# Kernel tuning notes

Measured on AMD Instinct MI355X. Metric: run time of the kernel, lower is better.

## Reference

```python
import jax, jax.numpy as jnp
import numpy as np

HEADS = 4
HID = 128
NEG_SLOPE = 0.2
N_NODES = 20000
N_EDGES = 320000
N_GRAPHS = 64
IN_DIM = 12


def gat_layer(x, src, dst, W, a_src, a_dst, b, n):
    # PyG GATConv, heads=4, concat=False (mean over heads), add_self_loops handled by caller.
    h = (x @ W).reshape(n, HEADS, HID)                      # [N,H,C]
    e_src = jnp.einsum('nhc,hc->nh', h, a_src)              # [N,H]
    e_dst = jnp.einsum('nhc,hc->nh', h, a_dst)
    e = jax.nn.leaky_relu(e_src[src] + e_dst[dst], NEG_SLOPE)  # [E,H]
    m = jax.lax.stop_gradient(jax.ops.segment_max(e, dst, num_segments=n))
    ex = jnp.exp(e - m[dst])
    denom = jax.ops.segment_sum(ex, dst, num_segments=n)    # [N,H]
    alpha = ex / denom[dst]                                 # edge softmax over incoming edges
    out = jax.ops.segment_sum(alpha[:, :, None] * h[src], dst, num_segments=n)  # [N,H,C]
    return out.mean(axis=1) + b                             # concat=False -> head mean, then bias


def setup_inputs() -> dict:
    key = jax.random.key(0)
    ks = jax.random.split(key, 20)
    def glorot(k, shape):
        lim = float(np.sqrt(6.0 / (shape[0] + shape[-1])))
        return jax.random.uniform(k, shape, jnp.float32, -lim, lim)
    inp = {
        'x': jax.random.normal(ks[0], (N_NODES, IN_DIM), jnp.float32),
        'edge_index': jax.random.randint(ks[1], (2, N_EDGES), 0, N_NODES, jnp.int64 if jax.config.jax_enable_x64 else jnp.int32),
        'batch': jnp.sort(jax.random.randint(ks[2], (N_NODES,), 0, N_GRAPHS)),
        'batch_size_tensor': jax.random.uniform(ks[3], (N_GRAPHS, 1), jnp.float32),
        # GAT layer 1
        'W1': glorot(ks[4], (IN_DIM, HEADS * HID)), 'as1': glorot(ks[5], (HEADS, HID)),
        'ad1': glorot(ks[6], (HEADS, HID)), 'b1': jnp.zeros((HID,), jnp.float32),
        # GAT layer 2
        'W2': glorot(ks[7], (HID, HEADS * HID)), 'as2': glorot(ks[8], (HEADS, HID)),
        'ad2': glorot(ks[9], (HEADS, HID)), 'b2': jnp.zeros((HID,), jnp.float32),
        # GAT layer 3
        'W3': glorot(ks[10], (HID, HEADS * HID)), 'as3': glorot(ks[11], (HEADS, HID)),
        'ad3': glorot(ks[12], (HEADS, HID)), 'b3': jnp.zeros((HID,), jnp.float32),
        # MLP: (128+1)->128->64->2
        'M1': glorot(ks[13], (HID + 1, HID)), 'mb1': jnp.zeros((HID,), jnp.float32),
        'M2': glorot(ks[14], (HID, HID // 2)), 'mb2': jnp.zeros((HID // 2,), jnp.float32),
        'M3': glorot(ks[15], (HID // 2, 2)), 'mb3': jnp.zeros((2,), jnp.float32),
    }
    return inp


def reference(x, edge_index, batch, batch_size_tensor,
              W1, as1, ad1, b1, W2, as2, ad2, b2, W3, as3, ad3, b3,
              M1, mb1, M2, mb2, M3, mb3):
    n = x.shape[0]
    loops = jnp.arange(n, dtype=edge_index.dtype)
    src = jnp.concatenate([edge_index[0], loops])   # add_self_loops=True (PyG default)
    dst = jnp.concatenate([edge_index[1], loops])
    h = jax.nn.relu(gat_layer(x, src, dst, W1, as1, ad1, b1, n))
    h = jax.nn.relu(gat_layer(h, src, dst, W2, as2, ad2, b2, n))
    h = jax.nn.relu(gat_layer(h, src, dst, W3, as3, ad3, b3, n))
    # global mean pool over graphs
    g = batch_size_tensor.shape[0]
    sums = jax.ops.segment_sum(h, batch, num_segments=g)
    cnts = jax.ops.segment_sum(jnp.ones((n,), h.dtype), batch, num_segments=g)
    pooled = sums / jnp.maximum(cnts, 1.0)[:, None]          # [G,128]
    bs = jnp.log1p(batch_size_tensor)                        # [G,1]
    z = jnp.concatenate([pooled, bs], axis=1)                # [G,129]
    z = jax.nn.relu(z @ M1 + mb1)                            # dropout(0.2) is identity at eval
    z = jax.nn.relu(z @ M2 + mb2)
    return z @ M3 + mb3                                      # [G,2]
```

## Files before the change

### kernel.cpp

```cpp
#include <hip/hip_runtime.h>
#include <hip/hip_bf16.h>
#include <math.h>

#define NN 20000
#define NE 320000
#define ET (NE + NN)
#define NG 64
#define HEADS 4
#define HID 128
#define OUTC (HEADS * HID)
#define SLOPE 0.2f

__device__ __forceinline__ float lrelu(float v) { return v > 0.f ? v : SLOPE * v; }

__global__ void k_hist(const int* __restrict__ ei, int* __restrict__ deg) {
  int e = blockIdx.x * blockDim.x + threadIdx.x;
  if (e >= ET) return;
  int dst = (e < NE) ? ei[NE + e] : (e - NE);
  atomicAdd(&deg[dst], 1);
}

__global__ void k_scan(const int* __restrict__ deg, int* __restrict__ row_start,
                       int* __restrict__ cursor) {
  __shared__ int sums[1024];
  int tid = threadIdx.x;
  const int PER = (NN + 1023) / 1024;
  int base = tid * PER;
  int local = 0;
  for (int i = 0; i < PER; ++i) { int idx = base + i; if (idx < NN) local += deg[idx]; }
  sums[tid] = local;
  __syncthreads();
  for (int off = 1; off < 1024; off <<= 1) {
    int v = (tid >= off) ? sums[tid - off] : 0;
    __syncthreads();
    sums[tid] += v;
    __syncthreads();
  }
  int run = sums[tid] - local;
  for (int i = 0; i < PER; ++i) {
    int idx = base + i;
    if (idx < NN) { row_start[idx] = run; cursor[idx] = run; run += deg[idx]; }
  }
  if (tid == 1023) row_start[NN] = sums[1023];
}

__global__ void k_scatter(const int* __restrict__ ei, int* __restrict__ cursor,
                          int* __restrict__ csr_src) {
  int e = blockIdx.x * blockDim.x + threadIdx.x;
  if (e >= ET) return;
  int src, dst;
  if (e < NE) { src = ei[e]; dst = ei[NE + e]; }
  else        { src = e - NE; dst = src; }
  int pos = atomicAdd(&cursor[dst], 1);
  csr_src[pos] = src;
}

__global__ void k_watt3(const float* __restrict__ W1, const float* __restrict__ as1,
                        const float* __restrict__ ad1, const float* __restrict__ W2,
                        const float* __restrict__ as2, const float* __restrict__ ad2,
                        const float* __restrict__ W3, const float* __restrict__ as3,
                        const float* __restrict__ ad3, float* __restrict__ watt1,
                        float* __restrict__ watt2, float* __restrict__ watt3) {
  int b = blockIdx.x;
  const float *W, *as, *ad;
  float* wo;
  int k;
  if (b < 12)       { k = b;       W = W1; as = as1; ad = ad1; wo = watt1; }
  else if (b < 140) { k = b - 12;  W = W2; as = as2; ad = ad2; wo = watt2; }
  else              { k = b - 140; W = W3; as = as3; ad = ad3; wo = watt3; }
  int tid = threadIdx.x;
  int t = tid & 7, h = t & 3;
  int c0 = (tid >> 3) * 4;
  const float* av = (t < 4 ? as : ad) + h * HID;
  const float* wr = W + (size_t)k * OUTC + h * HID;
  float4 wv = *reinterpret_cast<const float4*>(&wr[c0]);
  float4 a4 = *reinterpret_cast<const float4*>(&av[c0]);
  float p = wv.x * a4.x + wv.y * a4.y + wv.z * a4.z + wv.w * a4.w;
  __shared__ float lp[32][8];
  lp[tid >> 3][t] = p;
  __syncthreads();
  if (tid < 8) {
    float s = 0.f;
    for (int cc = 0; cc < 32; ++cc) s += lp[cc][tid];
    wo[k * 8 + tid] = s;
  }
}

__global__ void k_esd1(const float* __restrict__ x, const float* __restrict__ watt,
                       float* __restrict__ es, float* __restrict__ ed) {
  int n = blockIdx.x * blockDim.x + threadIdx.x;
  if (n >= NN) return;
  float xr[12];
#pragma unroll
  for (int k = 0; k < 12; ++k) xr[k] = x[(size_t)n * 12 + k];
#pragma unroll
  for (int t = 0; t < 8; ++t) {
    float acc = 0.f;
#pragma unroll
    for (int k = 0; k < 12; ++k) acc += xr[k] * watt[k * 8 + t];
    if (t < 4) es[n * 4 + t] = acc;
    else       ed[n * 4 + (t - 4)] = acc;
  }
}

__global__ void __launch_bounds__(256) k_esd128(
    const float* __restrict__ x, const float* __restrict__ watt,
    float* __restrict__ es, float* __restrict__ ed) {
  __shared__ float sw[HID * 8];
  int tid = threadIdx.x;
  for (int i = tid; i < HID * 8; i += 256) sw[i] = watt[i];
  __syncthreads();
  int local = tid >> 3;
  int t = tid & 7;
  int n = blockIdx.x * 32 + local;
  const float4* xr = reinterpret_cast<const float4*>(&x[(size_t)n * HID]);
  float acc = 0.f;
#pragma unroll 8
  for (int kq = 0; kq < 32; ++kq) {
    float4 xv = xr[kq];
    acc += xv.x * sw[(kq * 4 + 0) * 8 + t] + xv.y * sw[(kq * 4 + 1) * 8 + t]
         + xv.z * sw[(kq * 4 + 2) * 8 + t] + xv.w * sw[(kq * 4 + 3) * 8 + t];
  }
  if (t < 4) es[n * 4 + t] = acc;
  else       ed[n * 4 + (t - 4)] = acc;
}

__global__ void __launch_bounds__(256, 4) k_aggf(
    const float* __restrict__ x, const float* __restrict__ es,
    const float* __restrict__ ed, const int* __restrict__ row_start,
    const int* __restrict__ csr_src, float* __restrict__ z) {
  __shared__ float sal[4][256];
  int wid = threadIdx.x >> 6;
  int lane = threadIdx.x & 63;
  int n = blockIdx.x * 4 + wid;
  int start = row_start[n];
  int deg = row_start[n + 1] - start;
  const int* sp = csr_src + start;
  float4 edv = *reinterpret_cast<const float4*>(&ed[(size_t)n * 4]);
  int c = lane * 2;
  float2 a0c = make_float2(0.f, 0.f), a1c = make_float2(0.f, 0.f);
  float2 a2c = make_float2(0.f, 0.f), a3c = make_float2(0.f, 0.f);
  float d0 = 0.f, d1 = 0.f, d2 = 0.f, d3 = 0.f;
  for (int cb = 0; cb < deg; cb += 64) {
    int m = min(64, deg - cb);
    {
      int kk = cb + ((lane < m) ? lane : (m - 1));
      int s = sp[kk];
      float4 e4 = *reinterpret_cast<const float4*>(&es[(size_t)s * 4]);
      float4 ex;
      ex.x = __expf(lrelu(e4.x + edv.x));
      ex.y = __expf(lrelu(e4.y + edv.y));
      ex.z = __expf(lrelu(e4.z + edv.z));
      ex.w = __expf(lrelu(e4.w + edv.w));
      if (lane < m) {
        *reinterpret_cast<float4*>(&sal[wid][lane * 4]) = ex;
        d0 += ex.x; d1 += ex.y; d2 += ex.z; d3 += ex.w;
      }
    }
    asm volatile("s_waitcnt lgkmcnt(0)" ::: "memory");
    int j = 0;
    for (; j + 4 <= m; j += 4) {
      float4 q0 = *reinterpret_cast<const float4*>(&sal[wid][(j + 0) * 4]);
      float4 q1 = *reinterpret_cast<const float4*>(&sal[wid][(j + 1) * 4]);
      float4 q2 = *reinterpret_cast<const float4*>(&sal[wid][(j + 2) * 4]);
      float4 q3 = *reinterpret_cast<const float4*>(&sal[wid][(j + 3) * 4]);
      int s0 = sp[cb + j + 0], s1 = sp[cb + j + 1];
      int s2 = sp[cb + j + 2], s3 = sp[cb + j + 3];
      float2 x0 = *reinterpret_cast<const float2*>(&x[(size_t)s0 * HID + c]);
      float2 x1 = *reinterpret_cast<const float2*>(&x[(size_t)s1 * HID + c]);
      float2 x2 = *reinterpret_cast<const float2*>(&x[(size_t)s2 * HID + c]);
      float2 x3 = *reinterpret_cast<const float2*>(&x[(size_t)s3 * HID + c]);
      a0c.x += q0.x * x0.x; a0c.y += q0.x * x0.y;
      a1c.x += q0.y * x0.x; a1c.y += q0.y * x0.y;
      a2c.x += q0.z * x0.x; a2c.y += q0.z * x0.y;
      a3c.x += q0.w * x0.x; a3c.y += q0.w * x0.y;
      a0c.x += q1.x * x1.x; a0c.y += q1.x * x1.y;
      a1c.x += q1.y * x1.x; a1c.y += q1.y * x1.y;
      a2c.x += q1.z * x1.x; a2c.y += q1.z * x1.y;
      a3c.x += q1.w * x1.x; a3c.y += q1.w * x1.y;
      a0c.x += q2.x * x2.x; a0c.y += q2.x * x2.y;
      a1c.x += q2.y * x2.x; a1c.y += q2.y * x2.y;
      a2c.x += q2.z * x2.x; a2c.y += q2.z * x2.y;
      a3c.x += q2.w * x2.x; a3c.y += q2.w * x2.y;
      a0c.x += q3.x * x3.x; a0c.y += q3.x * x3.y;
      a1c.x += q3.y * x3.x; a1c.y += q3.y * x3.y;
      a2c.x += q3.z * x3.x; a2c.y += q3.z * x3.y;
      a3c.x += q3.w * x3.x; a3c.y += q3.w * x3.y;
    }
    for (; j < m; ++j) {
      float4 q = *reinterpret_cast<const float4*>(&sal[wid][j * 4]);
      int s = sp[cb + j];
      float2 xv = *reinterpret_cast<const float2*>(&x[(size_t)s * HID + c]);
      a0c.x += q.x * xv.x; a0c.y += q.x * xv.y;
      a1c.x += q.y * xv.x; a1c.y += q.y * xv.y;
      a2c.x += q.z * xv.x; a2c.y += q.z * xv.y;
      a3c.x += q.w * xv.x; a3c.y += q.w * xv.y;
    }
  }
#pragma unroll
  for (int off = 1; off < 64; off <<= 1) {
    d0 += __shfl_xor(d0, off);
    d1 += __shfl_xor(d1, off);
    d2 += __shfl_xor(d2, off);
    d3 += __shfl_xor(d3, off);
  }
  float i0 = 0.25f / d0, i1 = 0.25f / d1, i2 = 0.25f / d2, i3 = 0.25f / d3;
  a0c.x *= i0; a0c.y *= i0;
  a1c.x *= i1; a1c.y *= i1;
  a2c.x *= i2; a2c.y *= i2;
  a3c.x *= i3; a3c.y *= i3;
  float* zr = z + (size_t)n * OUTC;
  *reinterpret_cast<float2*>(&zr[0 * HID + c]) = a0c;
  *reinterpret_cast<float2*>(&zr[1 * HID + c]) = a1c;
  *reinterpret_cast<float2*>(&zr[2 * HID + c]) = a2c;
  *reinterpret_cast<float2*>(&zr[3 * HID + c]) = a3c;
}

__global__ void __launch_bounds__(256, 4) k_aggf1(
    const float* __restrict__ x, const float* __restrict__ es,
    const float* __restrict__ ed, const int* __restrict__ row_start,
    const int* __restrict__ csr_src, float* __restrict__ z1) {
  __shared__ float sal[4][256];
  int wid = threadIdx.x >> 6;
  int lane = threadIdx.x & 63;
  int n = blockIdx.x * 4 + wid;
  int start = row_start[n];
  int deg = row_start[n + 1] - start;
  const int* sp = csr_src + start;
  float4 edv = *reinterpret_cast<const float4*>(&ed[(size_t)n * 4]);
  int h = lane >> 4;
  int cr = lane & 15;
  int cc = cr < 12 ? cr : 11;
  float acc = 0.f;
  float d0 = 0.f, d1 = 0.f, d2 = 0.f, d3 = 0.f;
  for (int cb = 0; cb < deg; cb += 64) {
    int m = min(64, deg - cb);
    {
      int kk = cb + ((lane < m) ? lane : (m - 1));
      int s = sp[kk];
      float4 e4 = *reinterpret_cast<const float4*>(&es[(size_t)s * 4]);
      float4 ex;
      ex.x = __expf(lrelu(e4.x + edv.x));
      ex.y = __expf(lrelu(e4.y + edv.y));
      ex.z = __expf(lrelu(e4.z + edv.z));
      ex.w = __expf(lrelu(e4.w + edv.w));
      if (lane < m) {
        *reinterpret_cast<float4*>(&sal[wid][lane * 4]) = ex;
        d0 += ex.x; d1 += ex.y; d2 += ex.z; d3 += ex.w;
      }
    }
    asm volatile("s_waitcnt lgkmcnt(0)" ::: "memory");
    int j = 0;
    for (; j + 4 <= m; j += 4) {
      float ah0 = sal[wid][(j + 0) * 4 + h];
      float ah1 = sal[wid][(j + 1) * 4 + h];
      float ah2 = sal[wid][(j + 2) * 4 + h];
      float ah3 = sal[wid][(j + 3) * 4 + h];
      int s0 = sp[cb + j + 0], s1 = sp[cb + j + 1];
      int s2 = sp[cb + j + 2], s3 = sp[cb + j + 3];
      float x0 = x[(size_t)s0 * 12 + cc];
      float x1 = x[(size_t)s1 * 12 + cc];
      float x2 = x[(size_t)s2 * 12 + cc];
      float x3 = x[(size_t)s3 * 12 + cc];
      acc += ah0 * x0 + ah1 * x1 + ah2 * x2 + ah3 * x3;
    }
    for (; j < m; ++j) {
      float ah = sal[wid][j * 4 + h];
      int s = sp[cb + j];
      acc += ah * x[(size_t)s * 12 + cc];
    }
  }
#pragma unroll
  for (int off = 1; off < 64; off <<= 1) {
    d0 += __shfl_xor(d0, off);
    d1 += __shfl_xor(d1, off);
    d2 += __shfl_xor(d2, off);
    d3 += __shfl_xor(d3, off);
  }
  float dh = (h == 0) ? d0 : (h == 1) ? d1 : (h == 2) ? d2 : d3;
  float ivh = 0.25f / dh;
  if (cr < 12) z1[(size_t)n * 48 + h * 12 + cr] = acc * ivh;
}

template <int KTOT, int KH, int BK>
__global__ void k_gemm_full(const float* __restrict__ z, const float* __restrict__ W,
                            const float* __restrict__ bias, float* __restrict__ xout) {
  const int BM = 64, BN = 64;
  __shared__ float sAT[BK][BM + 4];
  __shared__ float sB[BK][BN];
  int tid = threadIdx.x;
  int r0 = blockIdx.y * BM;
  int cb = blockIdx.x * BN;
  int tx = tid & 15, ty = tid >> 4;
  int m0 = ty * 4, n0 = tx * 4;
  float acc[4][4] = {};
  for (int k0 = 0; k0 < KTOT; k0 += BK) {
    const int AF4 = BM * BK / 4;
    for (int idx = tid; idx < AF4; idx += 256) {
      int r = idx / (BK / 4);
      int kq = idx % (BK / 4);
      int row = r0 + r;
      float4 v = make_float4(0.f, 0.f, 0.f, 0.f);
      if (row < NN) v = *reinterpret_cast<const float4*>(&z[(size_t)row * KTOT + k0 + kq * 4]);
      sAT[kq * 4 + 0][r] = v.x;
      sAT[kq * 4 + 1][r] = v.y;
      sAT[kq * 4 + 2][r] = v.z;
      sAT[kq * 4 + 3][r] = v.w;
    }
    const int BF4 = BK * BN / 4;
    for (int idx = tid; idx < BF4; idx += 256) {
      int kr = idx / 16, nq = idx & 15;
      int kk = k0 + kr;
      int h = kk / KH, k = kk % KH;
      float4 v = *reinterpret_cast<const float4*>(&W[(size_t)k * OUTC + h * HID + cb + nq * 4]);
      *reinterpret_cast<float4*>(&sB[kr][nq * 4]) = v;
    }
    __syncthreads();
#pragma unroll 4
    for (int kk = 0; kk < BK; ++kk) {
      float4 a = *reinterpret_cast<const float4*>(&sAT[kk][m0]);
      float4 b = *reinterpret_cast<const float4*>(&sB[kk][n0]);
      acc[0][0] += a.x * b.x; acc[0][1] += a.x * b.y; acc[0][2] += a.x * b.z; acc[0][3] += a.x * b.w;
      acc[1][0] += a.y * b.x; acc[1][1] += a.y * b.y; acc[1][2] += a.y * b.z; acc[1][3] += a.y * b.w;
      acc[2][0] += a.z * b.x; acc[2][1] += a.z * b.y; acc[2][2] += a.z * b.z; acc[2][3] += a.z * b.w;
      acc[3][0] += a.w * b.x; acc[3][1] += a.w * b.y; acc[3][2] += a.w * b.z; acc[3][3] += a.w * b.w;
    }
    __syncthreads();
  }
  float4 bv = *reinterpret_cast<const float4*>(&bias[cb + n0]);
#pragma unroll
  for (int i = 0; i < 4; ++i) {
    int row = r0 + m0 + i;
    if (row < NN) {
      float4 o;
      o.x = fmaxf(acc[i][0] + bv.x, 0.f);
      o.y = fmaxf(acc[i][1] + bv.y, 0.f);
      o.z = fmaxf(acc[i][2] + bv.z, 0.f);
      o.w = fmaxf(acc[i][3] + bv.w, 0.f);
      *reinterpret_cast<float4*>(&xout[(size_t)row * HID + cb + n0]) = o;
    }
  }
}

template <int KTOT, int KH, int BK, int KCH>
__global__ void k_gemm_ks(const float* __restrict__ z, const float* __restrict__ W,
                          float* __restrict__ part) {
  const int BM = 64, BN = 128;
  __shared__ float sAT[BK][BM + 4];
  __shared__ float sB[BK][BN];
  int tid = threadIdx.x;
  int r0 = blockIdx.y * BM;
  int kc = blockIdx.z;
  int tx = tid & 15, ty = tid >> 4;
  int m0 = ty * 4, n0 = tx * 4;
  float acc0[4][4] = {};
  float acc1[4][4] = {};
  for (int k0 = kc * KCH; k0 < (kc + 1) * KCH; k0 += BK) {
    const int AF4 = BM * BK / 4;
    for (int idx = tid; idx < AF4; idx += 256) {
      int r = idx / (BK / 4);
      int kq = idx % (BK / 4);
      int row = r0 + r;
      float4 v = make_float4(0.f, 0.f, 0.f, 0.f);
      if (row < NN) v = *reinterpret_cast<const float4*>(&z[(size_t)row * KTOT + k0 + kq * 4]);
      sAT[kq * 4 + 0][r] = v.x;
      sAT[kq * 4 + 1][r] = v.y;
      sAT[kq * 4 + 2][r] = v.z;
      sAT[kq * 4 + 3][r] = v.w;
    }
    const int BF4 = BK * BN / 4;
    for (int idx = tid; idx < BF4; idx += 256) {
      int kr = idx >> 5, nq = idx & 31;
      int kk = k0 + kr;
      int h = kk / KH, k = kk % KH;
      float4 v = *reinterpret_cast<const float4*>(&W[(size_t)k * OUTC + h * HID + nq * 4]);
      *reinterpret_cast<float4*>(&sB[kr][nq * 4]) = v;
    }
    __syncthreads();
#pragma unroll 4
    for (int kk = 0; kk < BK; ++kk) {
      float4 a = *reinterpret_cast<const float4*>(&sAT[kk][m0]);
      float4 b0 = *reinterpret_cast<const float4*>(&sB[kk][n0]);
      float4 b1 = *reinterpret_cast<const float4*>(&sB[kk][64 + n0]);
      acc0[0][0] += a.x * b0.x; acc0[0][1] += a.x * b0.y; acc0[0][2] += a.x * b0.z; acc0[0][3] += a.x * b0.w;
      acc0[1][0] += a.y * b0.x; acc0[1][1] += a.y * b0.y; acc0[1][2] += a.y * b0.z; acc0[1][3] += a.y * b0.w;
      acc0[2][0] += a.z * b0.x; acc0[2][1] += a.z * b0.y; acc0[2][2] += a.z * b0.z; acc0[2][3] += a.z * b0.w;
      acc0[3][0] += a.w * b0.x; acc0[3][1] += a.w * b0.y; acc0[3][2] += a.w * b0.z; acc0[3][3] += a.w * b0.w;
      acc1[0][0] += a.x * b1.x; acc1[0][1] += a.x * b1.y; acc1[0][2] += a.x * b1.z; acc1[0][3] += a.x * b1.w;
      acc1[1][0] += a.y * b1.x; acc1[1][1] += a.y * b1.y; acc1[1][2] += a.y * b1.z; acc1[1][3] += a.y * b1.w;
      acc1[2][0] += a.z * b1.x; acc1[2][1] += a.z * b1.y; acc1[2][2] += a.z * b1.z; acc1[2][3] += a.z * b1.w;
      acc1[3][0] += a.w * b1.x; acc1[3][1] += a.w * b1.y; acc1[3][2] += a.w * b1.z; acc1[3][3] += a.w * b1.w;
    }
    __syncthreads();
  }
#pragma unroll
  for (int i = 0; i < 4; ++i) {
    int row = r0 + m0 + i;
    if (row < NN) {
      float4 v0 = make_float4(acc0[i][0], acc0[i][1], acc0[i][2], acc0[i][3]);
      float4 v1 = make_float4(acc1[i][0], acc1[i][1], acc1[i][2], acc1[i][3]);
      float* pr = &part[((size_t)kc * NN + row) * HID];
      *reinterpret_cast<float4*>(&pr[n0]) = v0;
      *reinterpret_cast<float4*>(&pr[64 + n0]) = v1;
    }
  }
}

template <int POOL, int NKC>
__global__ void k_epi(const float* __restrict__ part, const float* __restrict__ bias,
                      const int* __restrict__ batch, float* __restrict__ xout,
                      float* __restrict__ gsums) {
  int tid = threadIdx.x;
  int row = blockIdx.x * 2 + (tid >> 7);
  int c = tid & 127;
  float o = bias[c];
#pragma unroll
  for (int kc = 0; kc < NKC; ++kc)
    o += part[((size_t)kc * NN + row) * HID + c];
  o = fmaxf(o, 0.f);
  if (POOL) {
    atomicAdd(&gsums[(size_t)batch[row] * HID + c], o);
  } else {
    xout[(size_t)row * HID + c] = o;
  }
}

__global__ void k_mlp(const float* __restrict__ sums, const int* __restrict__ batch,
                      const float* __restrict__ bst, const float* __restrict__ M1,
                      const float* __restrict__ mb1, const float* __restrict__ M2,
                      const float* __restrict__ mb2, const float* __restrict__ M3,
                      const float* __restrict__ mb3, float* __restrict__ out) {
  int g = blockIdx.x, tid = threadIdx.x;
  int lo = 0, hi = NN;
  while (lo < hi) { int mid = (lo + hi) >> 1; if (batch[mid] < g) lo = mid + 1; else hi = mid; }
  int s = lo;
  lo = s; hi = NN;
  while (lo < hi) { int mid = (lo + hi) >> 1; if (batch[mid] < g + 1) lo = mid + 1; else hi = mid; }
  int e = lo;
  float cnt = (float)(e - s);
  float pooled = sums[g * HID + tid] / fmaxf(cnt, 1.f);
  __shared__ float z[HID + 1];
  __shared__ float z1[HID];
  __shared__ float z2[64];
  z[tid] = pooled;
  if (tid == 0) z[HID] = log1pf(bst[g]);
  __syncthreads();
  float a1 = mb1[tid];
  for (int k = 0; k < HID + 1; ++k) a1 += z[k] * M1[k * HID + tid];
  z1[tid] = a1 > 0.f ? a1 : 0.f;
  __syncthreads();
  if (tid < 64) {
    float a2 = mb2[tid];
    for (int k = 0; k < HID; ++k) a2 += z1[k] * M2[k * 64 + tid];
    z2[tid] = a2 > 0.f ? a2 : 0.f;
  }
  __syncthreads();
  if (tid < 2) {
    float a3 = mb3[tid];
    for (int k = 0; k < 64; ++k) a3 += z2[k] * M3[k * 2 + tid];
    out[g * 2 + tid] = a3;
  }
}

extern "C" void kernel_launch(void* const* d_in, const int* in_sizes, int n_in,
                              void* d_out, int out_size, void* d_ws, size_t ws_size,
                              hipStream_t stream) {
  const float* x   = (const float*)d_in[0];
  const int*   ei  = (const int*)d_in[1];
  const int*   bat = (const int*)d_in[2];
  const float* bst = (const float*)d_in[3];
  const float* W1 = (const float*)d_in[4];
  const float* as1 = (const float*)d_in[5];
  const float* ad1 = (const float*)d_in[6];
  const float* b1 = (const float*)d_in[7];
  const float* W2 = (const float*)d_in[8];
  const float* as2 = (const float*)d_in[9];
  const float* ad2 = (const float*)d_in[10];
  const float* b2 = (const float*)d_in[11];
  const float* W3 = (const float*)d_in[12];
  const float* as3 = (const float*)d_in[13];
  const float* ad3 = (const float*)d_in[14];
  const float* b3 = (const float*)d_in[15];
  const float* M1 = (const float*)d_in[16];
  const float* mb1 = (const float*)d_in[17];
  const float* M2 = (const float*)d_in[18];
  const float* mb2 = (const float*)d_in[19];
  const float* M3 = (const float*)d_in[20];
  const float* mb3 = (const float*)d_in[21];
  float* out = (float*)d_out;

  const bool use4 = ws_size >= (size_t)110 * 1024 * 1024;

  char* ws = (char*)d_ws;
  auto alloc = [&](size_t bytes) -> void* {
    void* p = (void*)ws;
    ws += (bytes + 255) & ~(size_t)255;
    return p;
  };
  float* z_buf  = (float*)alloc((size_t)NN * OUTC * 4);
  float* z1_buf = (float*)alloc((size_t)NN * 48 * 4);
  float* x_buf  = (float*)alloc((size_t)NN * HID * 4);
  float* e_src  = (float*)alloc((size_t)NN * 4 * 4);
  float* e_dst  = (float*)alloc((size_t)NN * 4 * 4);
  int*   deg    = (int*)alloc((size_t)NN * 4);
  int*   rowst  = (int*)alloc((size_t)(NN + 1) * 4);
  int*   cursor = (int*)alloc((size_t)NN * 4);
  int*   csr    = (int*)alloc((size_t)ET * 4);
  float* part   = (float*)alloc((size_t)(use4 ? 4 : 2) * NN * HID * 4);
  float* watt1  = (float*)alloc((size_t)12 * 8 * 4);
  float* watt2  = (float*)alloc((size_t)HID * 8 * 4);
  float* watt3  = (float*)alloc((size_t)HID * 8 * 4);
  float* gsums  = (float*)alloc((size_t)NG * HID * 4);

  hipMemsetAsync(deg, 0, (size_t)NN * 4, stream);
  hipMemsetAsync(gsums, 0, (size_t)NG * HID * 4, stream);
  k_hist<<<(ET + 255) / 256, 256, 0, stream>>>(ei, deg);
  k_scan<<<1, 1024, 0, stream>>>(deg, rowst, cursor);
  k_scatter<<<(ET + 255) / 256, 256, 0, stream>>>(ei, cursor, csr);
  k_watt3<<<268, 256, 0, stream>>>(W1, as1, ad1, W2, as2, ad2, W3, as3, ad3,
                                   watt1, watt2, watt3);

  dim3 pgrid(NN / 4);
  dim3 g1grid(2, (NN + 63) / 64);
  dim3 ks4grid(1, (NN + 63) / 64, 4);
  dim3 ks2grid(1, (NN + 63) / 64, 2);
  dim3 epigrid(NN / 2);
  k_esd1<<<(NN + 255) / 256, 256, 0, stream>>>(x, watt1, e_src, e_dst);
  k_aggf1<<<pgrid, 256, 0, stream>>>(x, e_src, e_dst, rowst, csr, z1_buf);
  k_gemm_full<48, 12, 48><<<g1grid, 256, 0, stream>>>(z1_buf, W1, b1, x_buf);
  k_esd128<<<NN / 32, 256, 0, stream>>>(x_buf, watt2, e_src, e_dst);
  k_aggf<<<pgrid, 256, 0, stream>>>(x_buf, e_src, e_dst, rowst, csr, z_buf);
  if (use4) {
    k_gemm_ks<512, 128, 32, 128><<<ks4grid, 256, 0, stream>>>(z_buf, W2, part);
    k_epi<0, 4><<<epigrid, 256, 0, stream>>>(part, b2, bat, x_buf, gsums);
  } else {
    k_gemm_ks<512, 128, 32, 256><<<ks2grid, 256, 0, stream>>>(z_buf, W2, part);
    k_epi<0, 2><<<epigrid, 256, 0, stream>>>(part, b2, bat, x_buf, gsums);
  }
  k_esd128<<<NN / 32, 256, 0, stream>>>(x_buf, watt3, e_src, e_dst);
  k_aggf<<<pgrid, 256, 0, stream>>>(x_buf, e_src, e_dst, rowst, csr, z_buf);
  if (use4) {
    k_gemm_ks<512, 128, 32, 128><<<ks4grid, 256, 0, stream>>>(z_buf, W3, part);
    k_epi<1, 4><<<epigrid, 256, 0, stream>>>(part, b3, bat, x_buf, gsums);
  } else {
    k_gemm_ks<512, 128, 32, 256><<<ks2grid, 256, 0, stream>>>(z_buf, W3, part);
    k_epi<1, 2><<<epigrid, 256, 0, stream>>>(part, b3, bat, x_buf, gsums);
  }
  k_mlp<<<NG, 128, 0, stream>>>(gsums, bat, bst, M1, mb1, M2, mb2, M3, mb3, out);
}
```

Measured before the change: 321.4 us.

## Fuse layer-2 epilogue with attention-score projection and add 8-way split-K path

Adds k_epi_esd, which reduces the split-K partials, applies bias and ReLU, writes the node features, and computes the per-node source/destination attention scores for the next layer from shared memory. This removes the separate k_esd128 launch and its re-read of x_buf. It also adds an 8-way split-K GEMM variant, chosen when the workspace is large enough, to raise parallelism at the cost of more partial-sum traffic in the epilogue. Only 8 of 256 threads per block do the score dot products, which may serialise the tail of that kernel.

```diff
diff --git a/kernel.cpp b/kernel.cpp
--- a/kernel.cpp
+++ b/kernel.cpp
@@ -425,6 +425,34 @@
   }
 }
 
+template <int NKC>
+__global__ void k_epi_esd(const float* __restrict__ part, const float* __restrict__ bias,
+                          float* __restrict__ xout, const float* __restrict__ watt,
+                          float* __restrict__ es, float* __restrict__ ed) {
+  __shared__ float sx[2][HID];
+  int tid = threadIdx.x;
+  int slot = tid >> 7;
+  int row = blockIdx.x * 2 + slot;
+  int c = tid & 127;
+  float o = bias[c];
+#pragma unroll
+  for (int kc = 0; kc < NKC; ++kc)
+    o += part[((size_t)kc * NN + row) * HID + c];
+  o = fmaxf(o, 0.f);
+  xout[(size_t)row * HID + c] = o;
+  sx[slot][c] = o;
+  __syncthreads();
+  int t = tid & 127;
+  if (t < 8) {
+    int r = blockIdx.x * 2 + slot;
+    float acc = 0.f;
+#pragma unroll 16
+    for (int k = 0; k < HID; ++k) acc += sx[slot][k] * watt[k * 8 + t];
+    if (t < 4) es[r * 4 + t] = acc;
+    else       ed[r * 4 + (t - 4)] = acc;
+  }
+}
+
 __global__ void k_mlp(const float* __restrict__ sums, const int* __restrict__ batch,
                       const float* __restrict__ bst, const float* __restrict__ M1,
                       const float* __restrict__ mb1, const float* __restrict__ M2,
@@ -489,7 +517,9 @@
   const float* mb3 = (const float*)d_in[21];
   float* out = (float*)d_out;
 
-  const bool use4 = ws_size >= (size_t)110 * 1024 * 1024;
+  const bool use8 = ws_size >= (size_t)170 * 1024 * 1024;
+  const bool use4 = !use8 && ws_size >= (size_t)110 * 1024 * 1024;
+  const int nkc = use8 ? 8 : (use4 ? 4 : 2);
 
   char* ws = (char*)d_ws;
   auto alloc = [&](size_t bytes) -> void* {
@@ -506,7 +536,7 @@
   int*   rowst  = (int*)alloc((size_t)(NN + 1) * 4);
   int*   cursor = (int*)alloc((size_t)NN * 4);
   int*   csr    = (int*)alloc((size_t)ET * 4);
-  float* part   = (float*)alloc((size_t)(use4 ? 4 : 2) * NN * HID * 4);
+  float* part   = (float*)alloc((size_t)nkc * NN * HID * 4);
   float* watt1  = (float*)alloc((size_t)12 * 8 * 4);
   float* watt2  = (float*)alloc((size_t)HID * 8 * 4);
   float* watt3  = (float*)alloc((size_t)HID * 8 * 4);
@@ -522,6 +552,7 @@
 
   dim3 pgrid(NN / 4);
   dim3 g1grid(2, (NN + 63) / 64);
+  dim3 ks8grid(1, (NN + 63) / 64, 8);
   dim3 ks4grid(1, (NN + 63) / 64, 4);
   dim3 ks2grid(1, (NN + 63) / 64, 2);
   dim3 epigrid(NN / 2);
@@ -530,16 +561,21 @@
   k_gemm_full<48, 12, 48><<<g1grid, 256, 0, stream>>>(z1_buf, W1, b1, x_buf);
   k_esd128<<<NN / 32, 256, 0, stream>>>(x_buf, watt2, e_src, e_dst);
   k_aggf<<<pgrid, 256, 0, stream>>>(x_buf, e_src, e_dst, rowst, csr, z_buf);
-  if (use4) {
+  if (use8) {
+    k_gemm_ks<512, 128, 32, 64><<<ks8grid, 256, 0, stream>>>(z_buf, W2, part);
+    k_epi_esd<8><<<epigrid, 256, 0, stream>>>(part, b2, x_buf, watt3, e_src, e_dst);
+  } else if (use4) {
     k_gemm_ks<512, 128, 32, 128><<<ks4grid, 256, 0, stream>>>(z_buf, W2, part);
-    k_epi<0, 4><<<epigrid, 256, 0, stream>>>(part, b2, bat, x_buf, gsums);
+    k_epi_esd<4><<<epigrid, 256, 0, stream>>>(part, b2, x_buf, watt3, e_src, e_dst);
   } else {
     k_gemm_ks<512, 128, 32, 256><<<ks2grid, 256, 0, stream>>>(z_buf, W2, part);
-    k_epi<0, 2><<<epigrid, 256, 0, stream>>>(part, b2, bat, x_buf, gsums);
-  }
-  k_esd128<<<NN / 32, 256, 0, stream>>>(x_buf, watt3, e_src, e_dst);
+    k_epi_esd<2><<<epigrid, 256, 0, stream>>>(part, b2, x_buf, watt3, e_src, e_dst);
+  }
   k_aggf<<<pgrid, 256, 0, stream>>>(x_buf, e_src, e_dst, rowst, csr, z_buf);
-  if (use4) {
+  if (use8) {
+    k_gemm_ks<512, 128, 32, 64><<<ks8grid, 256, 0, stream>>>(z_buf, W3, part);
+    k_epi<1, 8><<<epigrid, 256, 0, stream>>>(part, b3, bat, x_buf, gsums);
+  } else if (use4) {
     k_gemm_ks<512, 128, 32, 128><<<ks4grid, 256, 0, stream>>>(z_buf, W3, part);
     k_epi<1, 4><<<epigrid, 256, 0, stream>>>(part, b3, bat, x_buf, gsums);
   } else {
```

After: 330.7 us. 1.03x slower.
